# Kernel optimization log

Measured on AMD Instinct MI355X. Metric: run time of the kernel, lower is better.

## Reference

```python
import jax, jax.numpy as jnp
import numpy as np
from jax import lax

V, E, H, T, B = 32000, 512, 512, 64, 64

def _xavier(key, shape):
    fan_out, fan_in = shape
    std = np.sqrt(2.0 / (fan_in + fan_out))
    return jax.random.normal(key, shape, dtype=jnp.float32) * std

def setup_inputs() -> dict:
    key = jax.random.key(0)
    ks = jax.random.split(key, 12)
    scale = np.sqrt(3.0 / E)
    emb = jax.random.uniform(ks[0], (V, E), minval=-scale, maxval=scale, dtype=jnp.float32)
    return {
        "emb": emb,                                   # frozen embedding table [V,E]
        "W_ih": _xavier(ks[1], (3 * H, E)),           # GRU input weights (r,z,n stacked)
        "W_hh": _xavier(ks[2], (3 * H, H)),           # GRU hidden weights
        "b_ih": jnp.zeros((3 * H,), jnp.float32),
        "b_hh": jnp.zeros((3 * H,), jnp.float32),
        "zt_W": _xavier(ks[3], (H, E + H)), "zt_b": jnp.zeros((H,), jnp.float32),
        "rt_W": _xavier(ks[4], (E, E + H)), "rt_b": jnp.zeros((E,), jnp.float32),
        "ht_W": _xavier(ks[5], (H, E + H)), "ht_b": jnp.zeros((H,), jnp.float32),
        "dec_W": _xavier(ks[6], (V, H)), "dec_b": jnp.zeros((V,), jnp.float32),
        "init_hidden": jnp.zeros((1, B, H), jnp.float32),
        "word": jax.random.randint(ks[7], (B,), 0, V),
        "seq": jax.random.randint(ks[8], (T, B), 0, V),
    }

def reference(emb, W_ih, W_hh, b_ih, b_hh, zt_W, zt_b, rt_W, rt_b, ht_W, ht_b,
              dec_W, dec_b, init_hidden, word, seq):
    word_emb = emb[word]          # [B,E] (frozen)
    seq_emb = emb[seq]            # [T,B,E]
    h0 = init_hidden[0]           # [B,H], single layer

    def step(h, x):
        # standard torch GRU cell
        gi = x @ W_ih.T + b_ih    # [B,3H]
        gh = h @ W_hh.T + b_hh
        i_r, i_z, i_n = jnp.split(gi, 3, axis=-1)
        h_r, h_z, h_n = jnp.split(gh, 3, axis=-1)
        r = jax.nn.sigmoid(i_r + h_r)
        z = jax.nn.sigmoid(i_z + h_z)
        n = jnp.tanh(i_n + r * h_n)
        h_gru = (1.0 - z) * n + z * h      # rnn output at this step
        # extra GRU-style gating with word embedding (use_g branch)
        inp_h = jnp.concatenate([word_emb, h_gru], axis=-1)      # [B,E+H]
        zt = jax.nn.sigmoid(inp_h @ zt_W.T + zt_b)               # [B,H]
        rt = jax.nn.sigmoid(inp_h @ rt_W.T + rt_b)               # [B,E]
        hcat = jnp.concatenate([rt * word_emb, h_gru], axis=-1)  # [B,E+H]
        h_tilde = jnp.tanh(hcat @ ht_W.T + ht_b)                 # [B,H]
        h_new = (1.0 - zt) * h_gru + zt * h_tilde
        return h_new, h_gru

    h_final, outs = lax.scan(step, h0, seq_emb)   # outs [T,B,H]
    flat = outs.reshape(-1, H)                    # [T*B,H]
    decoded = flat @ dec_W.T + dec_b              # [T*B,V]
    return decoded, h_final[None]                 # hidden [1,B,H]
```

## Files before the change

kernel.cpp:

```cpp
#include <hip/hip_runtime.h>
#include <stdint.h>

#define GAS __attribute__((address_space(1)))
#define LAS __attribute__((address_space(3)))

typedef __bf16 bf16x8 __attribute__((ext_vector_type(8)));
typedef _Float16 f16x8 __attribute__((ext_vector_type(8)));
typedef float f32x4 __attribute__((ext_vector_type(4)));
typedef unsigned u32x4 __attribute__((ext_vector_type(4)));

__device__ __forceinline__ unsigned short f2bf(float f) {
  unsigned u = __float_as_uint(f);
  unsigned r = (u + 0x7FFFu + ((u >> 16) & 1u)) >> 16;
  return (unsigned short)r;
}

__device__ __forceinline__ float sigmoidf(float x) {
  return 1.f / (1.f + expf(-x));
}

__device__ __forceinline__ void st2c(_Float16* p, _Float16 v) {
  unsigned short u = __builtin_bit_cast(unsigned short, v);
  __hip_atomic_store((unsigned short*)p, u, __ATOMIC_RELAXED, __HIP_MEMORY_SCOPE_AGENT);
}
__device__ __forceinline__ void stf_mall(unsigned* p, unsigned v) {
  __hip_atomic_store(p, v, __ATOMIC_RELAXED, __HIP_MEMORY_SCOPE_AGENT);
}
__device__ __forceinline__ unsigned ldf_mall(const unsigned* p) {
  return __hip_atomic_load(p, __ATOMIC_RELAXED, __HIP_MEMORY_SCOPE_AGENT);
}
template <int OFF>
__device__ __forceinline__ f16x8 ldh8_mall(const _Float16* p) {
  u32x4 r;
  asm volatile("global_load_dwordx4 %0, %1, off offset:%2 sc0 sc1"
               : "=v"(r) : "v"(p), "n"(OFF) : "memory");
  return __builtin_bit_cast(f16x8, r);
}

__global__ __launch_bounds__(128) void k_gather(
    const float* __restrict__ emb, const int* __restrict__ seq,
    const int* __restrict__ word, unsigned short* __restrict__ xbf,
    float* __restrict__ wemb) {
  int row = blockIdx.x;
  int tid = threadIdx.x;
  if (row < 4096) {
    const float* src = emb + (size_t)seq[row] * 512;
    unsigned short* dst = xbf + (size_t)row * 512;
    for (int e = tid; e < 512; e += 128) dst[e] = f2bf(src[e]);
  } else {
    int b = row - 4096;
    const float* src = emb + (size_t)word[b] * 512;
    float* dst = wemb + (size_t)b * 512;
    for (int e = tid; e < 512; e += 128) dst[e] = src[e];
  }
}

__global__ __launch_bounds__(128) void k_conv(
    const float* __restrict__ Wih, const float* __restrict__ decW,
    unsigned short* __restrict__ wih_bf, unsigned short* __restrict__ dec_bf) {
  int row = blockIdx.x;
  int tid = threadIdx.x;
  if (row < 1536) {
    const float* s = Wih + (size_t)row * 512;
    unsigned short* d = wih_bf + (size_t)row * 512;
    for (int e = tid; e < 512; e += 128) d[e] = f2bf(s[e]);
  } else {
    int o = row - 1536;
    const float* s = decW + (size_t)o * 512;
    unsigned short* d = dec_bf + (size_t)o * 512;
    for (int e = tid; e < 512; e += 128) d[e] = f2bf(s[e]);
  }
}

__global__ __launch_bounds__(256) void k_pre(
    const float* __restrict__ ztW, const float* __restrict__ ztb,
    const float* __restrict__ rtW, const float* __restrict__ rtb,
    const float* __restrict__ wemb, float* __restrict__ ztp,
    float* __restrict__ rtp) {
  int idx = blockIdx.x * 256 + threadIdx.x;
  int b = idx >> 10, o = idx & 1023;
  const float4* we = (const float4*)(wemb + (size_t)b * 512);
  const float4* wr;
  float acc;
  if (o < 512) { wr = (const float4*)(ztW + (size_t)o * 1024); acc = ztb[o]; }
  else { wr = (const float4*)(rtW + (size_t)(o - 512) * 1024); acc = rtb[o - 512]; }
  for (int c = 0; c < 128; ++c) {
    float4 w = wr[c], e = we[c];
    acc += w.x * e.x + w.y * e.y + w.z * e.z + w.w * e.w;
  }
  if (o < 512) ztp[(size_t)b * 512 + o] = acc;
  else rtp[(size_t)b * 512 + (o - 512)] = acc;
}

__global__ __launch_bounds__(256) void k_gemm_bt(
    const unsigned short* __restrict__ A, const unsigned short* __restrict__ B,
    float* __restrict__ C, const float* __restrict__ bias,
    int M, int N, int K) {
  __shared__ __align__(16) unsigned short As[128 * 32];
  __shared__ __align__(16) unsigned short Bs[128 * 32];
  int nt = N >> 7;
  int nwg = gridDim.x;
  int bid = blockIdx.x;
  int swz = (bid & 7) * (nwg >> 3) + (bid >> 3);
  int m0 = (swz / nt) << 7, n0 = (swz % nt) << 7;
  int tid = threadIdx.x;
  int l = tid & 63, w = tid >> 6;
  int wr = w >> 1, wc = w & 1;
  int lr = l & 15, lk = l >> 4;
  f32x4 acc[4][4] = {};
  for (int k0 = 0; k0 < K; k0 += 32) {
#pragma unroll
    for (int i = 0; i < 2; ++i) {
      int c = w * 2 + i;
      int off = c * 1024 + l * 16;
      int row = off >> 6, kb = off & 63;
      const char* ga = (const char*)A + ((size_t)(m0 + row) * K + k0) * 2 + kb;
      const char* gb = (const char*)B + ((size_t)(n0 + row) * K + k0) * 2 + kb;
      __builtin_amdgcn_global_load_lds((const GAS void*)ga,
                                       (LAS void*)((char*)As + c * 1024), 16, 0, 0);
      __builtin_amdgcn_global_load_lds((const GAS void*)gb,
                                       (LAS void*)((char*)Bs + c * 1024), 16, 0, 0);
    }
    asm volatile("s_waitcnt vmcnt(0)" ::: "memory");
    __syncthreads();
    bf16x8 af[4], bfr[4];
#pragma unroll
    for (int i = 0; i < 4; ++i)
      af[i] = *(const bf16x8*)&As[(wr * 64 + i * 16 + lr) * 32 + lk * 8];
#pragma unroll
    for (int i = 0; i < 4; ++i)
      bfr[i] = *(const bf16x8*)&Bs[(wc * 64 + i * 16 + lr) * 32 + lk * 8];
#pragma unroll
    for (int i = 0; i < 4; ++i)
#pragma unroll
      for (int jj = 0; jj < 4; ++jj)
        acc[i][jj] = __builtin_amdgcn_mfma_f32_16x16x32_bf16(af[i], bfr[jj], acc[i][jj], 0, 0, 0);
    __syncthreads();
  }
#pragma unroll
  for (int jj = 0; jj < 4; ++jj) {
    int col = n0 + wc * 64 + jj * 16 + lr;
    float bv = bias ? bias[col] : 0.f;
#pragma unroll
    for (int i = 0; i < 4; ++i) {
      int rb = m0 + wr * 64 + i * 16 + lk * 4;
#pragma unroll
      for (int q = 0; q < 4; ++q)
        C[(size_t)(rb + q) * N + col] = acc[i][jj][q] + bv;
    }
  }
}

struct RnnP {
  const float *Whh, *ztW, *rtW, *htW;
  const float *gi, *ztp, *rtp, *wemb, *inith, *bhh, *htb;
  _Float16 *hcurF, *hgruF, *rwF;
  unsigned short *outsb;
  float *hfin;
  unsigned *flags;
};

__device__ __forceinline__ void poll_band(const unsigned* flags, int w, int l,
                                          unsigned tgt) {
  const unsigned* fp = flags + ((size_t)((l & 31) * 4 + w)) * 16;
  for (;;) {
    unsigned v = ldf_mall(fp);
    if (__all((int)(v >= tgt))) break;
  }
}

template <int NT>
__device__ __forceinline__ void mm_mall(f32x4* acc, const _Float16* A,
                                        const _Float16* WLrow, int w, int lr, int lk) {
  f16x8 af[16];
  const _Float16* arow = A + ((size_t)(16 * w + lr)) * 512 + lk * 8;
#define LDA(c) af[c] = ldh8_mall<(c) * 64>(arow);
  LDA(0) LDA(1) LDA(2) LDA(3) LDA(4) LDA(5) LDA(6) LDA(7)
  LDA(8) LDA(9) LDA(10) LDA(11) LDA(12) LDA(13) LDA(14) LDA(15)
#undef LDA
  asm volatile("s_waitcnt vmcnt(0)" ::: "memory");
  __builtin_amdgcn_sched_barrier(0);
#pragma unroll
  for (int c = 0; c < 16; ++c) {
#pragma unroll
    for (int n = 0; n < NT; ++n) {
      f16x8 bb = *(const f16x8*)(WLrow + (n * 16 + lr) * 520 + c * 32 + lk * 8);
      acc[n] = __builtin_amdgcn_mfma_f32_16x16x32_f16(af[c], bb, acc[n], 0, 0, 0);
    }
  }
}

__global__ __launch_bounds__(256) void k_rnn6(RnnP p) {
  const int g = blockIdx.x, tid = threadIdx.x;
  const int w = tid >> 6, l = tid & 63;
  const int lr = l & 15, lk = l >> 4;
  unsigned* myflag = p.flags + ((size_t)(g * 4 + w)) * 16;
  __shared__ _Float16 WL[112 * 520];
  for (int idx = tid; idx < 112 * 512; idx += 256) {
    int rr = idx >> 9, e = idx & 511;
    const float* src;
    if (rr < 48) {
      int gate = rr >> 4, i = rr & 15;
      src = p.Whh + ((size_t)(gate * 512 + g * 16 + i)) * 512 + e;
    } else if (rr < 96) {
      int r2 = rr - 48, gate = r2 >> 4, i = r2 & 15;
      const float* base = gate == 0 ? p.ztW : (gate == 1 ? p.rtW : p.htW);
      src = base + ((size_t)(g * 16 + i)) * 1024 + 512 + e;
    } else {
      int i = rr - 96;
      src = p.htW + ((size_t)(g * 16 + i)) * 1024 + e;
    }
    WL[rr * 520 + e] = (_Float16)(*src);
  }
  const int j = g * 16 + lr;
  const int brow = 16 * w + lk * 4;
  f32x4 hprev, zp, rp, wev;
#pragma unroll
  for (int q = 0; q < 4; ++q) {
    int b = brow + q;
    hprev[q] = p.inith[(size_t)b * 512 + j];
    zp[q] = p.ztp[(size_t)b * 512 + j];
    rp[q] = p.rtp[(size_t)b * 512 + j];
    wev[q] = p.wemb[(size_t)b * 512 + j];
    st2c(&p.hcurF[(size_t)b * 512 + j], (_Float16)hprev[q]);
  }
  const float br = p.bhh[j], bz = p.bhh[512 + j], bn = p.bhh[1024 + j];
  const float bht = p.htb[j];
  float gir[12];
#pragma unroll
  for (int q = 0; q < 4; ++q) {
    const float* git = p.gi + (size_t)(brow + q) * 1536;
    gir[q * 3 + 0] = git[j];
    gir[q * 3 + 1] = git[512 + j];
    gir[q * 3 + 2] = git[1024 + j];
  }
  __syncthreads();
  if (l == 0) stf_mall(myflag, 1u);

  for (int t = 0; t < 64; ++t) {
    const unsigned base = 3u * (unsigned)t;
    poll_band(p.flags, w, l, base + 1);
    f32x4 acc1[3] = {};
    mm_mall<3>(acc1, p.hcurF, &WL[0], w, lr, lk);
    f32x4 hg;
#pragma unroll
    for (int q = 0; q < 4; ++q) {
      int b = brow + q;
      float r = sigmoidf(gir[q * 3 + 0] + br + acc1[0][q]);
      float z = sigmoidf(gir[q * 3 + 1] + bz + acc1[1][q]);
      float n = tanhf(gir[q * 3 + 2] + r * (acc1[2][q] + bn));
      float hgq = (1.f - z) * n + z * hprev[q];
      hg[q] = hgq;
      st2c(&p.hgruF[(size_t)b * 512 + j], (_Float16)hgq);
    }
    asm volatile("s_waitcnt vmcnt(0)" ::: "memory");
    if (l == 0) stf_mall(myflag, base + 2);
#pragma unroll
    for (int q = 0; q < 4; ++q)
      p.outsb[((size_t)t * 64 + brow + q) * 512 + j] = f2bf(hg[q]);
    if (t < 63) {
      const float* git = p.gi + (size_t)(t + 1) * 64 * 1536;
#pragma unroll
      for (int q = 0; q < 4; ++q) {
        const float* gb = git + (size_t)(brow + q) * 1536;
        gir[q * 3 + 0] = gb[j];
        gir[q * 3 + 1] = gb[512 + j];
        gir[q * 3 + 2] = gb[1024 + j];
      }
    }
    poll_band(p.flags, w, l, base + 2);
    f32x4 acc2[3] = {};
    mm_mall<3>(acc2, p.hgruF, &WL[48 * 520], w, lr, lk);
    f32x4 zt, htB;
#pragma unroll
    for (int q = 0; q < 4; ++q) {
      int b = brow + q;
      float ztq = sigmoidf(zp[q] + acc2[0][q]);
      float rtq = sigmoidf(rp[q] + acc2[1][q]);
      zt[q] = ztq;
      htB[q] = acc2[2][q];
      st2c(&p.rwF[(size_t)b * 512 + j], (_Float16)(rtq * wev[q]));
    }
    asm volatile("s_waitcnt vmcnt(0)" ::: "memory");
    if (l == 0) stf_mall(myflag, base + 3);
    poll_band(p.flags, w, l, base + 3);
    f32x4 acc3[1] = {};
    mm_mall<1>(acc3, p.rwF, &WL[96 * 520], w, lr, lk);
#pragma unroll
    for (int q = 0; q < 4; ++q) {
      int b = brow + q;
      float htl = tanhf(acc3[0][q] + htB[q] + bht);
      float hn2 = (1.f - zt[q]) * hg[q] + zt[q] * htl;
      hprev[q] = hn2;
      if (t < 63) st2c(&p.hcurF[(size_t)b * 512 + j], (_Float16)hn2);
      else p.hfin[(size_t)b * 512 + j] = hn2;
    }
    if (t < 63) {
      asm volatile("s_waitcnt vmcnt(0)" ::: "memory");
      if (l == 0) stf_mall(myflag, base + 4);
    }
  }
}

extern "C" void kernel_launch(void* const* d_in, const int* in_sizes, int n_in,
                              void* d_out, int out_size, void* d_ws, size_t ws_size,
                              hipStream_t stream) {
  const float* emb   = (const float*)d_in[0];
  const float* Wih   = (const float*)d_in[1];
  const float* Whh   = (const float*)d_in[2];
  const float* bih   = (const float*)d_in[3];
  const float* bhh   = (const float*)d_in[4];
  const float* ztW   = (const float*)d_in[5];
  const float* ztb   = (const float*)d_in[6];
  const float* rtW   = (const float*)d_in[7];
  const float* rtb   = (const float*)d_in[8];
  const float* htW   = (const float*)d_in[9];
  const float* htb   = (const float*)d_in[10];
  const float* decW  = (const float*)d_in[11];
  const float* decb  = (const float*)d_in[12];
  const float* inith = (const float*)d_in[13];
  const int* word    = (const int*)d_in[14];
  const int* seq     = (const int*)d_in[15];
  float* out = (float*)d_out;

  char* ws = (char*)d_ws;
  size_t off = 0;
  auto alloc = [&](size_t bytes) {
    size_t o = off;
    off += (bytes + 255) & ~(size_t)255;
    return o;
  };
  unsigned short* xbf   = (unsigned short*)(ws + alloc(4096ull * 512 * 2));
  unsigned short* wihbf = (unsigned short*)(ws + alloc(1536ull * 512 * 2));
  unsigned short* decbf = (unsigned short*)(ws + alloc(32000ull * 512 * 2));
  float* wemb           = (float*)(ws + alloc(64ull * 512 * 4));
  float* ztp            = (float*)(ws + alloc(64ull * 512 * 4));
  float* rtp            = (float*)(ws + alloc(64ull * 512 * 4));
  float* gi             = (float*)(ws + alloc(4096ull * 1536 * 4));
  unsigned short* outsb = (unsigned short*)(ws + alloc(4096ull * 512 * 2));
  _Float16* hcurF       = (_Float16*)(ws + alloc(64ull * 512 * 2));
  _Float16* hgruF       = (_Float16*)(ws + alloc(64ull * 512 * 2));
  _Float16* rwF         = (_Float16*)(ws + alloc(64ull * 512 * 2));
  unsigned* flags       = (unsigned*)(ws + alloc(128 * 64));

  hipLaunchKernelGGL(k_gather, dim3(4160), dim3(128), 0, stream,
                     emb, seq, word, xbf, wemb);
  hipLaunchKernelGGL(k_conv, dim3(33536), dim3(128), 0, stream,
                     Wih, decW, wihbf, decbf);
  hipLaunchKernelGGL(k_pre, dim3(256), dim3(256), 0, stream,
                     ztW, ztb, rtW, rtb, wemb, ztp, rtp);
  hipLaunchKernelGGL(k_gemm_bt, dim3(384), dim3(256), 0, stream,
                     xbf, wihbf, gi, bih, 4096, 1536, 512);
  hipMemsetAsync(flags, 0, 128 * 64, stream);
  RnnP p{Whh, ztW, rtW, htW, gi, ztp, rtp, wemb, inith, bhh, htb,
         hcurF, hgruF, rwF, outsb, out + 4096ull * 32000, flags};
  hipLaunchKernelGGL(k_rnn6, dim3(32), dim3(256), 0, stream, p);
  hipLaunchKernelGGL(k_gemm_bt, dim3(8000), dim3(256), 0, stream,
                     outsb, decbf, out, decb, 4096, 32000, 512);
}
```

Measured before the change: 1.270 ms.

## Replace full-barrier polling with incremental per-producer chunk consumption in RNN matmuls

Each matmul no longer waits for every producer block's flag before starting. It polls the flags, loads the K-chunks whose two producer blocks have already published, and folds those MFMAs in order while waiting for the rest. This overlaps the cross-block synchronisation latency with compute along the sequential recurrence. The cost is more complex control flow, repeated ballots and flag reads, and a dynamically indexed register array that may spill or serialise.

```diff
diff --git a/kernel.cpp b/kernel.cpp
--- a/kernel.cpp
+++ b/kernel.cpp
@@ -160,37 +160,45 @@
   unsigned *flags;
 };
 
-__device__ __forceinline__ void poll_band(const unsigned* flags, int w, int l,
-                                          unsigned tgt) {
+template <int NT>
+__device__ __forceinline__ void mm_inc(f32x4* acc, const _Float16* A,
+                                       const _Float16* WLrow, unsigned tgt,
+                                       int w, int l, int lr, int lk,
+                                       const unsigned* flags) {
+  f16x8 af[16] = {};
+  const _Float16* arow = A + ((size_t)(16 * w + lr)) * 512 + lk * 8;
   const unsigned* fp = flags + ((size_t)((l & 31) * 4 + w)) * 16;
-  for (;;) {
+  unsigned loaded = 0;
+  int folded = 0;
+  while (folded < 16) {
     unsigned v = ldf_mall(fp);
-    if (__all((int)(v >= tgt))) break;
-  }
-}
-
-template <int NT>
-__device__ __forceinline__ void mm_mall(f32x4* acc, const _Float16* A,
-                                        const _Float16* WLrow, int w, int lr, int lk) {
-  f16x8 af[16];
-  const _Float16* arow = A + ((size_t)(16 * w + lr)) * 512 + lk * 8;
-#define LDA(c) af[c] = ldh8_mall<(c) * 64>(arow);
-  LDA(0) LDA(1) LDA(2) LDA(3) LDA(4) LDA(5) LDA(6) LDA(7)
-  LDA(8) LDA(9) LDA(10) LDA(11) LDA(12) LDA(13) LDA(14) LDA(15)
-#undef LDA
-  asm volatile("s_waitcnt vmcnt(0)" ::: "memory");
-  __builtin_amdgcn_sched_barrier(0);
-#pragma unroll
-  for (int c = 0; c < 16; ++c) {
-#pragma unroll
-    for (int n = 0; n < NT; ++n) {
-      f16x8 bb = *(const f16x8*)(WLrow + (n * 16 + lr) * 520 + c * 32 + lk * 8);
-      acc[n] = __builtin_amdgcn_mfma_f32_16x16x32_f16(af[c], bb, acc[n], 0, 0, 0);
-    }
-  }
-}
-
-__global__ __launch_bounds__(256) void k_rnn6(RnnP p) {
+    unsigned rm = (unsigned)__ballot((int)(v >= tgt));
+    unsigned pr = rm & (rm >> 1) & 0x55555555u;
+    unsigned nl = pr & ~loaded;
+    if (nl) {
+#define LDP(p) if (nl & (1u << (2 * (p)))) af[p] = ldh8_mall<(p) * 64>(arow);
+      LDP(0) LDP(1) LDP(2) LDP(3) LDP(4) LDP(5) LDP(6) LDP(7)
+      LDP(8) LDP(9) LDP(10) LDP(11) LDP(12) LDP(13) LDP(14) LDP(15)
+#undef LDP
+      asm volatile("s_waitcnt vmcnt(0)" ::: "memory");
+      __builtin_amdgcn_sched_barrier(0);
+      loaded |= nl;
+    }
+#pragma unroll
+    for (int p = 0; p < 16; ++p) {
+      if (folded == p && ((loaded >> (2 * p)) & 1u)) {
+#pragma unroll
+        for (int n = 0; n < NT; ++n) {
+          f16x8 bb = *(const f16x8*)(WLrow + (n * 16 + lr) * 520 + p * 32 + lk * 8);
+          acc[n] = __builtin_amdgcn_mfma_f32_16x16x32_f16(af[p], bb, acc[n], 0, 0, 0);
+        }
+        folded = p + 1;
+      }
+    }
+  }
+}
+
+__global__ __launch_bounds__(256) void k_rnn8(RnnP p) {
   const int g = blockIdx.x, tid = threadIdx.x;
   const int w = tid >> 6, l = tid & 63;
   const int lr = l & 15, lk = l >> 4;
@@ -239,9 +247,8 @@
 
   for (int t = 0; t < 64; ++t) {
     const unsigned base = 3u * (unsigned)t;
-    poll_band(p.flags, w, l, base + 1);
     f32x4 acc1[3] = {};
-    mm_mall<3>(acc1, p.hcurF, &WL[0], w, lr, lk);
+    mm_inc<3>(acc1, p.hcurF, &WL[0], base + 1, w, l, lr, lk, p.flags);
     f32x4 hg;
 #pragma unroll
     for (int q = 0; q < 4; ++q) {
@@ -268,9 +275,8 @@
         gir[q * 3 + 2] = gb[1024 + j];
       }
     }
-    poll_band(p.flags, w, l, base + 2);
     f32x4 acc2[3] = {};
-    mm_mall<3>(acc2, p.hgruF, &WL[48 * 520], w, lr, lk);
+    mm_inc<3>(acc2, p.hgruF, &WL[48 * 520], base + 2, w, l, lr, lk, p.flags);
     f32x4 zt, htB;
 #pragma unroll
     for (int q = 0; q < 4; ++q) {
@@ -283,9 +289,8 @@
     }
     asm volatile("s_waitcnt vmcnt(0)" ::: "memory");
     if (l == 0) stf_mall(myflag, base + 3);
-    poll_band(p.flags, w, l, base + 3);
     f32x4 acc3[1] = {};
-    mm_mall<1>(acc3, p.rwF, &WL[96 * 520], w, lr, lk);
+    mm_inc<1>(acc3, p.rwF, &WL[96 * 520], base + 3, w, l, lr, lk, p.flags);
 #pragma unroll
     for (int q = 0; q < 4; ++q) {
       int b = brow + q;
@@ -354,7 +359,7 @@
   hipMemsetAsync(flags, 0, 128 * 64, stream);
   RnnP p{Whh, ztW, rtW, htW, gi, ztp, rtp, wemb, inith, bhh, htb,
          hcurF, hgruF, rwF, outsb, out + 4096ull * 32000, flags};
-  hipLaunchKernelGGL(k_rnn6, dim3(32), dim3(256), 0, stream, p);
+  hipLaunchKernelGGL(k_rnn8, dim3(32), dim3(256), 0, stream, p);
   hipLaunchKernelGGL(k_gemm_bt, dim3(8000), dim3(256), 0, stream,
                      outsb, decbf, out, decb, 4096, 32000, 512);
 }
```

New measurement: 1.409 ms. +10.9%, slower.

## Add specialized decoder GEMM with direct-to-LDS loads, swizzled LDS, and staged stores

Applied to the files above, without the earlier changes.

Replaces the generic GEMM for the 4096x32000x512 decoder projection with a dedicated kernel. It loads A and B tiles straight into LDS via global_load_lds with an XOR swizzle to avoid bank conflicts, uses a K-step of 64, and remaps workgroup IDs for L2 locality. The output goes through LDS in two halves so the fp32 result is written with coalesced float4 stores instead of scattered scalar stores. The staging adds extra barriers and LDS traffic in the epilogue, and there is no double buffering, so loads and MFMAs do not overlap.

```diff
diff --git a/kernel.cpp b/kernel.cpp
--- a/kernel.cpp
+++ b/kernel.cpp
@@ -147,6 +147,86 @@
 #pragma unroll
       for (int q = 0; q < 4; ++q)
         C[(size_t)(rb + q) * N + col] = acc[i][jj][q] + bv;
+    }
+  }
+}
+
+__global__ __launch_bounds__(256) void k_dec(
+    const unsigned short* __restrict__ A, const unsigned short* __restrict__ B,
+    float* __restrict__ C, const float* __restrict__ bias) {
+  __shared__ __align__(16) char LSD[64 * 132 * 4];
+  unsigned short* As = (unsigned short*)LSD;
+  unsigned short* Bs = (unsigned short*)(LSD + 16384);
+  float* Cst = (float*)LSD;
+  const int nt = 250;
+  int nwg = gridDim.x;
+  int bid = blockIdx.x;
+  int swz = (bid & 7) * (nwg >> 3) + (bid >> 3);
+  int m0 = (swz / nt) << 7, n0 = (swz % nt) << 7;
+  int tid = threadIdx.x;
+  int l = tid & 63, w = tid >> 6;
+  int wr = w >> 1, wc = w & 1;
+  int lr = l & 15, lk = l >> 4;
+  int srcswz = 16 * ((l & 7) ^ (l >> 3));
+  f32x4 acc[4][4] = {};
+  for (int k0 = 0; k0 < 512; k0 += 64) {
+#pragma unroll
+    for (int c = 0; c < 4; ++c) {
+      int row = (w * 4 + c) * 8 + (l >> 3);
+      const char* ga = (const char*)A + ((size_t)(m0 + row) * 512 + k0) * 2 + srcswz;
+      const char* gb = (const char*)B + ((size_t)(n0 + row) * 512 + k0) * 2 + srcswz;
+      __builtin_amdgcn_global_load_lds((const GAS void*)ga,
+          (LAS void*)((char*)As + (w * 4 + c) * 1024), 16, 0, 0);
+      __builtin_amdgcn_global_load_lds((const GAS void*)gb,
+          (LAS void*)((char*)Bs + (w * 4 + c) * 1024), 16, 0, 0);
+    }
+    asm volatile("s_waitcnt vmcnt(0)" ::: "memory");
+    __syncthreads();
+#pragma unroll
+    for (int h = 0; h < 2; ++h) {
+      bf16x8 af[4], bfr[4];
+#pragma unroll
+      for (int i = 0; i < 4; ++i) {
+        int rowa = wr * 64 + i * 16 + lr;
+        int offa = rowa * 128 + ((h * 64 + lk * 16) ^ ((rowa & 7) << 4));
+        af[i] = *(const bf16x8*)((const char*)As + offa);
+        int rowb = wc * 64 + i * 16 + lr;
+        int offb = rowb * 128 + ((h * 64 + lk * 16) ^ ((rowb & 7) << 4));
+        bfr[i] = *(const bf16x8*)((const char*)Bs + offb);
+      }
+#pragma unroll
+      for (int i = 0; i < 4; ++i)
+#pragma unroll
+        for (int jj = 0; jj < 4; ++jj)
+          acc[i][jj] = __builtin_amdgcn_mfma_f32_16x16x32_bf16(af[i], bfr[jj], acc[i][jj], 0, 0, 0);
+    }
+    __syncthreads();
+  }
+  float bv[4];
+#pragma unroll
+  for (int jj = 0; jj < 4; ++jj) bv[jj] = bias[n0 + wc * 64 + jj * 16 + lr];
+#pragma unroll 1
+  for (int ch = 0; ch < 2; ++ch) {
+    __syncthreads();
+    if (wr == ch) {
+#pragma unroll
+      for (int i = 0; i < 4; ++i)
+#pragma unroll
+        for (int jj = 0; jj < 4; ++jj)
+#pragma unroll
+          for (int q = 0; q < 4; ++q) {
+            int rl = i * 16 + lk * 4 + q;
+            int cl = wc * 64 + jj * 16 + lr;
+            Cst[rl * 132 + cl] = acc[i][jj][q] + bv[jj];
+          }
+    }
+    __syncthreads();
+#pragma unroll
+    for (int ps = 0; ps < 8; ++ps) {
+      int flat = (ps * 256 + tid) * 4;
+      int rl = flat >> 7, cl = flat & 127;
+      float4 v = *(const float4*)&Cst[rl * 132 + cl];
+      *(float4*)&C[(size_t)(m0 + ch * 64 + rl) * 32000 + n0 + cl] = v;
     }
   }
 }
@@ -355,6 +435,6 @@
   RnnP p{Whh, ztW, rtW, htW, gi, ztp, rtp, wemb, inith, bhh, htb,
          hcurF, hgruF, rwF, outsb, out + 4096ull * 32000, flags};
   hipLaunchKernelGGL(k_rnn6, dim3(32), dim3(256), 0, stream, p);
-  hipLaunchKernelGGL(k_gemm_bt, dim3(8000), dim3(256), 0, stream,
-                     outsb, decbf, out, decb, 4096, 32000, 512);
-}
+  hipLaunchKernelGGL(k_dec, dim3(8000), dim3(256), 0, stream,
+                     outsb, decbf, out, decb);
+}
```

After: 1.244 ms, median of 2. -2.1%, faster.
